# Performance work log

Measured on AMD Instinct MI355X. Metric: run time of the kernel, lower is better.

Reference implementation:

```python
import jax, jax.numpy as jnp
import numpy as np
import math

INPUT_DIM = 1024
EXPANSION = 4
SPARSITY = 0.15
ACT_SPARSITY = 0.1
OUTPUT_DIM = INPUT_DIM * EXPANSION
K = max(1, int(OUTPUT_DIM * ACT_SPARSITY))  # 409
BATCH = 16384


def setup_inputs() -> dict:
    key = jax.random.key(0)
    kx, kw, km = jax.random.split(key, 3)
    x = jax.random.normal(kx, (BATCH, INPUT_DIM), dtype=jnp.float32)
    # sparse random projection buffer, built exactly as in __init__
    w = jax.random.normal(kw, (OUTPUT_DIM, INPUT_DIM), dtype=jnp.float32)
    mask = (jax.random.uniform(km, (OUTPUT_DIM, INPUT_DIM)) < SPARSITY).astype(jnp.float32)
    scale = 1.5 / math.sqrt(INPUT_DIM * SPARSITY)
    projection_weights = w * mask * scale
    return {"x": x, "projection_weights": projection_weights}


def reference(x, projection_weights):
    # data-dependent bipolar rescale: torch uses `if x.min() >= 0`; express with where
    x_bipolar = jnp.where(x.min() >= 0, (x - 0.5) * 2.0, x)
    # [B, D_out] dense projection
    projected = jnp.einsum("bi,oi->bo", x_bipolar, projection_weights)
    # k-WTA: threshold at k-th largest value per row
    top_values, _ = jax.lax.top_k(projected, K)
    threshold = top_values[:, -1:]  # [B, 1]
    mask = (projected >= threshold).astype(projected.dtype)
    encoded = jax.nn.relu(projected) * mask
    # F.normalize(p=2, dim=1): divide by max(norm, eps)
    norm = jnp.sqrt(jnp.sum(encoded * encoded, axis=1, keepdims=True))
    return encoded / jnp.maximum(norm, 1e-12)
```

## Files before the change

kernel.cpp:

```cpp
#include <hip/hip_runtime.h>

#define BATCH   16384
#define IN_DIM  1024
#define OUT_DIM 4096
#define K_TOP   409
#define DELTA_W 6.5e-3f

typedef _Float16 half8  __attribute__((ext_vector_type(8)));
typedef _Float16 half4v __attribute__((ext_vector_type(4)));
typedef float    f32x4  __attribute__((ext_vector_type(4)));

#define WS_XH_OFF   256
#define WS_WH_OFF   (WS_XH_OFF + (size_t)BATCH * IN_DIM * 2)
#define WS_THR_OFF  (WS_WH_OFF + (size_t)OUT_DIM * IN_DIM * 2)
#define WS_CNT_OFF  (WS_THR_OFF + (size_t)BATCH * 8)
#define WS_COL_OFF  (WS_CNT_OFF + (size_t)BATCH * 8)
#define WS_NP_OFF   (WS_COL_OFF + (size_t)BATCH * 64 * 4)
#define WS_WV_OFF   (WS_NP_OFF + (size_t)BATCH * 64 * 4)
#define WS_WI_OFF   (WS_WV_OFF + (size_t)OUT_DIM * 256 * 4)
#define WS_WN_OFF   (WS_WI_OFF + (size_t)OUT_DIM * 256 * 2)
#define WS_NEEDED   (WS_WH_OFF + (size_t)OUT_DIM * IN_DIM * 2)
#define WS_NEED3    (WS_WN_OFF + (size_t)OUT_DIM * 4)


__global__ __launch_bounds__(256)
void k_hasneg(const float* __restrict__ x, int n, int* __restrict__ flag) {
    const int stride = gridDim.x * blockDim.x;
    bool neg = false;
    for (int i = blockIdx.x * blockDim.x + threadIdx.x; i < n; i += stride)
        neg |= (x[i] < 0.0f);
    unsigned long long b = __ballot(neg);
    if (b != 0ULL && (threadIdx.x & 63) == 0)
        atomicOr(flag, 1);
}

__global__ __launch_bounds__(256)
void k_cvt(const float* __restrict__ x, const float* __restrict__ w,
           _Float16* __restrict__ xh, _Float16* __restrict__ wh,
           const int* __restrict__ flag) {
    const bool bipolar = (*flag == 0);
    const int stride = gridDim.x * blockDim.x;
    const int nx4 = BATCH * IN_DIM / 4;
    const int nw4 = OUT_DIM * IN_DIM / 4;
    for (int i = blockIdx.x * blockDim.x + threadIdx.x; i < nx4; i += stride) {
        float4 v = ((const float4*)x)[i];
        if (bipolar) {
            v.x = (v.x - 0.5f) * 2.0f; v.y = (v.y - 0.5f) * 2.0f;
            v.z = (v.z - 0.5f) * 2.0f; v.w = (v.w - 0.5f) * 2.0f;
        }
        ((half4v*)xh)[i] = half4v{ (_Float16)v.x, (_Float16)v.y,
                                   (_Float16)v.z, (_Float16)v.w };
    }
    for (int i = blockIdx.x * blockDim.x + threadIdx.x; i < nw4; i += stride) {
        float4 u = ((const float4*)w)[i];
        ((half4v*)wh)[i] = half4v{ (_Float16)u.x, (_Float16)u.y,
                                   (_Float16)u.z, (_Float16)u.w };
    }
}

__global__ __launch_bounds__(256)
void k_wcomp(const float* __restrict__ w, float* __restrict__ wv,
             unsigned short* __restrict__ wi, int* __restrict__ wn) {
    const int lane = threadIdx.x & 63;
    const int row = blockIdx.x * 4 + (threadIdx.x >> 6);
    const float* wr = w + (size_t)row * IN_DIM;
    const float4* wr4 = (const float4*)(wr + lane * 16);
    float4 v[4];
    int cnt = 0;
    #pragma unroll
    for (int q = 0; q < 4; ++q) {
        v[q] = wr4[q];
        cnt += (v[q].x != 0.0f) + (v[q].y != 0.0f)
             + (v[q].z != 0.0f) + (v[q].w != 0.0f);
    }
    int off = cnt;
    #pragma unroll
    for (int d = 1; d < 64; d <<= 1) {
        int t = __shfl_up(off, d);
        if (lane >= d) off += t;
    }
    const int total = __shfl(off, 63);
    off -= cnt;
    float* dv = wv + (size_t)row * 256;
    unsigned short* di = wi + (size_t)row * 256;
    int pos = off;
    #pragma unroll
    for (int q = 0; q < 4; ++q) {
        #pragma unroll
        for (int e = 0; e < 4; ++e) {
            float f = (e == 0) ? v[q].x : (e == 1) ? v[q].y
                    : (e == 2) ? v[q].z : v[q].w;
            if (f != 0.0f) {
                dv[pos] = f;
                di[pos] = (unsigned short)(lane * 16 + q * 4 + e);
                ++pos;
            }
        }
    }
    if (lane == 0) {
        const int n4 = (total + 3) & ~3;
        for (int i = total; i < n4 && i < 256; ++i) { dv[i] = 0.0f; di[i] = 0; }
        wn[row] = total;
    }
}

__global__ __launch_bounds__(512, 2)
void k_gemm16(const _Float16* __restrict__ xh, const _Float16* __restrict__ wh,
              float* __restrict__ out) {
    __shared__ _Float16 Ah[2][256 * 64];
    __shared__ _Float16 Bh[2][256 * 64];
    const int tid = threadIdx.x;
    const int bm = blockIdx.x, bn = blockIdx.y;
    const int lane = tid & 63;
    const int wv = tid >> 6;
    const int wm = wv >> 2, wn = wv & 3;
    const int lr = lane & 15, lk = lane >> 4;

    const int srow = (lane >> 3);
    const int sslot = (lane & 7) ^ srow;
    f32x4 acc[8][4] = {};

    const _Float16* aS[4]; const _Float16* bS[4];
    int dOff[4];
    #pragma unroll
    for (int i = 0; i < 4; ++i) {
        const int rb = i * 64 + wv * 8;
        aS[i] = xh + (size_t)(bm * 256 + rb + srow) * IN_DIM + sslot * 8;
        bS[i] = wh + (size_t)(bn * 256 + rb + srow) * IN_DIM + sslot * 8;
        dOff[i] = rb * 64;
    }

    #pragma unroll
    for (int i = 0; i < 4; ++i) {
        __builtin_amdgcn_global_load_lds((const __attribute__((address_space(1))) void*)(aS[i]), (__attribute__((address_space(3))) void*)&Ah[0][dOff[i]], 16, 0, 0);
        __builtin_amdgcn_global_load_lds((const __attribute__((address_space(1))) void*)(bS[i]), (__attribute__((address_space(3))) void*)&Bh[0][dOff[i]], 16, 0, 0);
    }
    __syncthreads();

    int cur = 0;
    #pragma unroll 1
    for (int t = 0; t < 16; ++t) {
        if (t < 15) {
            const int kt = (t + 1) * 64;
            #pragma unroll
            for (int i = 0; i < 4; ++i) {
                __builtin_amdgcn_global_load_lds((const __attribute__((address_space(1))) void*)(aS[i] + kt), (__attribute__((address_space(3))) void*)&Ah[cur ^ 1][dOff[i]], 16, 0, 0);
                __builtin_amdgcn_global_load_lds((const __attribute__((address_space(1))) void*)(bS[i] + kt), (__attribute__((address_space(3))) void*)&Bh[cur ^ 1][dOff[i]], 16, 0, 0);
            }
        }
        #pragma unroll
        for (int h = 0; h < 2; ++h) {
            half8 bf[4];
            #pragma unroll
            for (int j = 0; j < 4; ++j) {
                const int rbv = wn * 64 + j * 16 + lr;
                const int sb = (h * 4 + lk) ^ (rbv & 7);
                bf[j] = *(const half8*)&Bh[cur][rbv * 64 + (sb << 3)];
            }
            #pragma unroll
            for (int hf = 0; hf < 2; ++hf) {
                half8 af[4];
                #pragma unroll
                for (int i = 0; i < 4; ++i) {
                    const int ra = wm * 128 + (hf * 4 + i) * 16 + lr;
                    const int sa = (h * 4 + lk) ^ (ra & 7);
                    af[i] = *(const half8*)&Ah[cur][ra * 64 + (sa << 3)];
                }
                #pragma unroll
                for (int i = 0; i < 4; ++i)
                    #pragma unroll
                    for (int j = 0; j < 4; ++j)
                        acc[hf * 4 + i][j] = __builtin_amdgcn_mfma_f32_16x16x32_f16(
                            af[i], bf[j], acc[hf * 4 + i][j], 0, 0, 0);
            }
        }
        __syncthreads();
        cur ^= 1;
    }
    #pragma unroll
    for (int i = 0; i < 8; ++i)
        #pragma unroll
        for (int j = 0; j < 4; ++j)
            #pragma unroll
            for (int q = 0; q < 4; ++q) {
                const int row = bm * 256 + wm * 128 + i * 16 + lk * 4 + q;
                const int col = bn * 256 + wn * 64 + j * 16 + lr;
                _Float16* fo = (_Float16*)((char*)out + (size_t)row * OUT_DIM * 4);
                fo[col] = (_Float16)acc[i][j][q];
            }
}

__global__ __launch_bounds__(256)
void k_sel1(const float* __restrict__ po, float2* __restrict__ thr,
            int2* __restrict__ cnt, int* __restrict__ rcol) {
    __shared__ unsigned int bins[256];
    __shared__ float fred[4];
    __shared__ unsigned int wsum[4];
    __shared__ int s_b, s_b2;
    __shared__ unsigned int s_hi, s_slot, s_hi1;
    const int row = blockIdx.x;
    const int tid = threadIdx.x;
    const int lane = tid & 63, wq = tid >> 6;
    const _Float16* fr = (const _Float16*)((const char*)po + (size_t)row * OUT_DIM * 4);

    half8 h0 = *(const half8*)&fr[tid * 8];
    half8 h1 = *(const half8*)&fr[2048 + tid * 8];
    float fv[16];
    float vmax = -1e30f;
    #pragma unroll
    for (int e = 0; e < 8; ++e) {
        fv[e] = (float)h0[e];
        fv[8 + e] = (float)h1[e];
        vmax = fmaxf(vmax, fmaxf(fv[e], fv[8 + e]));
    }
    #pragma unroll
    for (int off = 32; off > 0; off >>= 1)
        vmax = fmaxf(vmax, __shfl_xor(vmax, off));
    if (lane == 0) fred[wq] = vmax;
    bins[tid] = 0;
    if (tid == 0) { s_hi = 0; s_slot = 0; s_b = 0; s_b2 = 0; s_hi1 = 0; }
    __syncthreads();
    vmax = fmaxf(fmaxf(fmaxf(fred[0], fred[1]), fmaxf(fred[2], fred[3])), 1e-6f);
    const float scale1 = 256.0f / vmax;
    const float invscale1 = vmax * (1.0f / 256.0f);

    #pragma unroll
    for (int e = 0; e < 16; ++e) {
        float f = fv[e];
        if (f > 0.0f) {
            int b = (int)(f * scale1);
            if (b > 255) b = 255;
            atomicAdd(&bins[b], 1u);
        }
    }
    __syncthreads();
    {
        const unsigned int c = bins[255 - tid];
        unsigned int sc = c;
        #pragma unroll
        for (int off = 1; off < 64; off <<= 1) {
            unsigned int t2 = __shfl_up(sc, off);
            if (lane >= off) sc += t2;
        }
        if (lane == 63) wsum[wq] = sc;
        __syncthreads();
        for (int q = 0; q < wq; ++q) sc += wsum[q];
        if ((int)sc >= K_TOP && (int)(sc - c) < K_TOP) {
            s_b = 255 - tid;
            s_hi1 = sc - c;
        }
    }
    __syncthreads();
    const int b1 = s_b;
    const unsigned int hi1 = s_hi1;
    const float blo = (float)b1 * invscale1;
    const float scale2 = scale1 * 256.0f;
    const float s2w = invscale1 * (1.0f / 256.0f);

    bins[tid] = 0;
    __syncthreads();
    #pragma unroll
    for (int e = 0; e < 16; ++e) {
        float f = fv[e];
        if (f > 0.0f) {
            int b = (int)(f * scale1);
            if (b > 255) b = 255;
            if (b == b1) {
                int b2 = (int)((f - blo) * scale2);
                if (b2 < 0) b2 = 0;
                if (b2 > 255) b2 = 255;
                atomicAdd(&bins[b2], 1u);
            }
        }
    }
    __syncthreads();
    {
        const unsigned int c = bins[255 - tid];
        unsigned int sc = c;
        #pragma unroll
        for (int off = 1; off < 64; off <<= 1) {
            unsigned int t2 = __shfl_up(sc, off);
            if (lane >= off) sc += t2;
        }
        if (lane == 63) wsum[wq] = sc;
        __syncthreads();
        for (int q = 0; q < wq; ++q) sc += wsum[q];
        if ((int)(hi1 + sc) >= K_TOP && (int)(hi1 + sc - c) < K_TOP)
            s_b2 = 255 - tid;
    }
    __syncthreads();
    const float thi = blo + (float)(s_b2 + 1) * s2w + DELTA_W;
    const float tlo = blo + (float)s_b2 * s2w - DELTA_W;

    #pragma unroll
    for (int e = 0; e < 16; ++e) {
        float f = fv[e];
        if (f > thi) atomicAdd(&s_hi, 1u);
        else if (f >= tlo) {
            unsigned int p = atomicAdd(&s_slot, 1u);
            const int j = (e < 8) ? (tid * 8 + e) : (2048 + tid * 8 + e - 8);
            if (p < 64) rcol[row * 64 + p] = j;
        }
    }
    __syncthreads();
    if (tid == 0) {
        int nb = (int)s_slot;
        int krem = K_TOP - (int)s_hi;
        if (krem > nb) krem = nb;
        if (krem < 0) krem = 0;
        thr[row] = make_float2(thi, tlo);
        cnt[row] = make_int2(nb, krem);
    }
}

__global__ __launch_bounds__(256)
void k_sel2(const float* __restrict__ x, const float* __restrict__ wvals,
            const unsigned short* __restrict__ widx, const int* __restrict__ wn,
            const int2* __restrict__ cnt, const int* __restrict__ rcol,
            float* __restrict__ rnp, const int* __restrict__ flag) {
    __shared__ float xs[4][IN_DIM];
    const int tid = threadIdx.x;
    const int lane = tid & 63;
    const int wv = tid >> 6;
    const int row = blockIdx.x * 4 + wv;
    const bool bipolar = (*flag == 0);

    const float4* xr4 = (const float4*)(x + (size_t)row * IN_DIM);
    #pragma unroll
    for (int u = 0; u < 4; ++u) {
        float4 xv = xr4[lane + 64 * u];
        if (bipolar) {
            xv.x = __fmul_rn(__fadd_rn(xv.x, -0.5f), 2.0f);
            xv.y = __fmul_rn(__fadd_rn(xv.y, -0.5f), 2.0f);
            xv.z = __fmul_rn(__fadd_rn(xv.z, -0.5f), 2.0f);
            xv.w = __fmul_rn(__fadd_rn(xv.w, -0.5f), 2.0f);
        }
        ((float4*)xs[wv])[lane + 64 * u] = xv;
    }
    __syncthreads();

    int nb = cnt[row].x; if (nb > 64) nb = 64;
    if (lane < nb) {
        const int col = rcol[row * 64 + lane];
        const int n4 = (wn[col] + 3) >> 2;
        const float4* v4 = (const float4*)(wvals + (size_t)col * 256);
        const ushort4* i4 = (const ushort4*)(widx + (size_t)col * 256);
        const float* xr = xs[wv];
        float p = 0.0f;
        #pragma unroll 2
        for (int i = 0; i < n4; ++i) {
            float4 vv = v4[i];
            ushort4 ii = i4[i];
            p = __fmaf_rn(xr[ii.x], vv.x, p);
            p = __fmaf_rn(xr[ii.y], vv.y, p);
            p = __fmaf_rn(xr[ii.z], vv.z, p);
            p = __fmaf_rn(xr[ii.w], vv.w, p);
        }
        rnp[row * 64 + lane] = p;
    }
}

__global__ __launch_bounds__(256)
void k_sel2_full(const float* __restrict__ x, const float* __restrict__ w,
                 const int2* __restrict__ cnt, const int* __restrict__ rcol,
                 float* __restrict__ rnp, const int* __restrict__ flag) {
    __shared__ float xs[4][IN_DIM];
    const int tid = threadIdx.x;
    const int lane = tid & 63;
    const int wv = tid >> 6;
    const int row = blockIdx.x * 4 + wv;
    const bool bipolar = (*flag == 0);

    const float4* xr4 = (const float4*)(x + (size_t)row * IN_DIM);
    #pragma unroll
    for (int u = 0; u < 4; ++u) {
        float4 xv = xr4[lane + 64 * u];
        if (bipolar) {
            xv.x = __fmul_rn(__fadd_rn(xv.x, -0.5f), 2.0f);
            xv.y = __fmul_rn(__fadd_rn(xv.y, -0.5f), 2.0f);
            xv.z = __fmul_rn(__fadd_rn(xv.z, -0.5f), 2.0f);
            xv.w = __fmul_rn(__fadd_rn(xv.w, -0.5f), 2.0f);
        }
        ((float4*)xs[wv])[lane + 64 * u] = xv;
    }
    __syncthreads();

    int nb = cnt[row].x; if (nb > 64) nb = 64;
    if (lane < nb) {
        const int col = rcol[row * 64 + lane];
        const float4* wr4 = (const float4*)(w + (size_t)col * IN_DIM);
        const float4* xs4 = (const float4*)xs[wv];
        float p = 0.0f;
        #pragma unroll 4
        for (int i = 0; i < IN_DIM / 4; ++i) {
            float4 xv = xs4[i];
            float4 wvv = wr4[i];
            p = __fmaf_rn(xv.x, wvv.x, p);
            p = __fmaf_rn(xv.y, wvv.y, p);
            p = __fmaf_rn(xv.z, wvv.z, p);
            p = __fmaf_rn(xv.w, wvv.w, p);
        }
        rnp[row * 64 + lane] = p;
    }
}

__global__ __launch_bounds__(256)
void k_sel3(float* __restrict__ po, const float2* __restrict__ thr,
            const int2* __restrict__ cnt, const int* __restrict__ rcol,
            const float* __restrict__ rnp) {
    __shared__ int bcol[64];
    __shared__ float bnp[64];
    __shared__ unsigned char bsel[64];
    __shared__ float fred[4];
    const int row = blockIdx.x;
    const int tid = threadIdx.x;
    const int lane = tid & 63, wq = tid >> 6;
    const float2 th = thr[row];
    const int2 cn = cnt[row];
    const float thi = th.x, tlo = th.y;
    const int nb = cn.x, krem = cn.y;
    const int nbc = nb > 64 ? 64 : nb;
    const bool need = (nb != krem);

    const _Float16* fr = (const _Float16*)((const char*)po + (size_t)row * OUT_DIM * 4);
    half8 h0 = *(const half8*)&fr[tid * 8];
    half8 h1 = *(const half8*)&fr[2048 + tid * 8];

    if (tid < nbc) { bcol[tid] = rcol[row * 64 + tid]; bnp[tid] = rnp[row * 64 + tid]; }
    __syncthreads();
    if (tid < nbc) {
        const float v = bnp[tid];
        int gc = 0;
        for (int l = 0; l < nbc; ++l) gc += (bnp[l] > v);
        bsel[tid] = (gc < krem) ? 1 : 0;
    }
    __syncthreads();

    float ov[16];
    float nrm2 = 0.0f;
    #pragma unroll
    for (int e = 0; e < 16; ++e) {
        float f = (e < 8) ? (float)h0[e] : (float)h1[e - 8];
        const int j = (e < 8) ? (tid * 8 + e) : (2048 + tid * 8 + e - 8);
        bool sel = (f > thi);
        float val = f;
        if (!sel && f >= tlo) {
            if (!need) sel = true;
            else {
                for (int m = 0; m < nbc; ++m)
                    if (bcol[m] == j) {
                        sel = (bsel[m] != 0);
                        val = bnp[m];
                        break;
                    }
            }
        }
        float eo = (sel && val > 0.0f) ? val : 0.0f;
        ov[e] = eo;
        nrm2 += eo * eo;
    }
    #pragma unroll
    for (int off = 32; off > 0; off >>= 1)
        nrm2 += __shfl_xor(nrm2, off);
    if (lane == 0) fred[wq] = nrm2;
    __syncthreads();
    const float total = fred[0] + fred[1] + fred[2] + fred[3];
    const float inv = 1.0f / fmaxf(sqrtf(total), 1e-12f);

    float4* p4 = (float4*)(po + (size_t)row * OUT_DIM);
    #pragma unroll
    for (int h = 0; h < 2; ++h) {
        const int base = (h == 0) ? 0 : 8;
        const int fi = (h == 0) ? (tid * 2) : (512 + tid * 2);
        float4 o0 = make_float4(ov[base + 0] * inv, ov[base + 1] * inv,
                                ov[base + 2] * inv, ov[base + 3] * inv);
        float4 o1 = make_float4(ov[base + 4] * inv, ov[base + 5] * inv,
                                ov[base + 6] * inv, ov[base + 7] * inv);
        p4[fi] = o0;
        p4[fi + 1] = o1;
    }
}

extern "C" void kernel_launch(void* const* d_in, const int* in_sizes, int n_in,
                              void* d_out, int out_size, void* d_ws, size_t ws_size,
                              hipStream_t stream) {
    const float* x = (const float*)d_in[0];
    const float* w = (const float*)d_in[1];
    float* out = (float*)d_out;
    int* flag = (int*)d_ws;

    hipMemsetAsync(flag, 0, sizeof(int), stream);
    k_hasneg<<<2048, 256, 0, stream>>>(x, BATCH * IN_DIM, flag);

    dim3 g(BATCH / 256, OUT_DIM / 256);
    _Float16* xh = (_Float16*)((char*)d_ws + WS_XH_OFF);
    _Float16* wh = (_Float16*)((char*)d_ws + WS_WH_OFF);
    k_cvt<<<2048, 256, 0, stream>>>(x, w, xh, wh, flag);
    k_gemm16<<<g, 512, 0, stream>>>(xh, wh, out);

    float2* thr = (float2*)((char*)d_ws + WS_THR_OFF);
    int2*   cnt = (int2*)((char*)d_ws + WS_CNT_OFF);
    int*    rcol = (int*)((char*)d_ws + WS_COL_OFF);
    float*  rnp = (float*)((char*)d_ws + WS_NP_OFF);
    k_sel1<<<BATCH, 256, 0, stream>>>(out, thr, cnt, rcol);
    if (ws_size >= WS_NEED3) {
        float* wv = (float*)((char*)d_ws + WS_WV_OFF);
        unsigned short* wi = (unsigned short*)((char*)d_ws + WS_WI_OFF);
        int* wn = (int*)((char*)d_ws + WS_WN_OFF);
        k_wcomp<<<OUT_DIM / 4, 256, 0, stream>>>(w, wv, wi, wn);
        k_sel2<<<BATCH / 4, 256, 0, stream>>>(x, wv, wi, wn, cnt, rcol, rnp, flag);
    } else {
        k_sel2_full<<<BATCH / 4, 256, 0, stream>>>(x, w, cnt, rcol, rnp, flag);
    }
    k_sel3<<<BATCH, 256, 0, stream>>>(out, thr, cnt, rcol, rnp);
}
```

Baseline: 450.9 us.

## Fuse selection stages into one per-row kernel and merge conversion with weight compaction

Three post-GEMM kernels (threshold histogram, borderline fp32 recompute, final mask/normalize) are merged into a single per-row kernel. The fp16 row stays in registers and the candidate column lists stay in shared memory instead of going through workspace arrays. The conversion kernel now also builds the compacted sparse weight rows, which removes a separate launch. This saves two row re-reads and several launches per call. In exchange the fused kernel has a larger shared-memory footprint and divergent branches, and the borderline dot products now run one row per block instead of packing four rows per block.

```diff
diff --git a/kernel.cpp b/kernel.cpp
--- a/kernel.cpp
+++ b/kernel.cpp
@@ -12,14 +12,10 @@
 
 #define WS_XH_OFF   256
 #define WS_WH_OFF   (WS_XH_OFF + (size_t)BATCH * IN_DIM * 2)
-#define WS_THR_OFF  (WS_WH_OFF + (size_t)OUT_DIM * IN_DIM * 2)
-#define WS_CNT_OFF  (WS_THR_OFF + (size_t)BATCH * 8)
-#define WS_COL_OFF  (WS_CNT_OFF + (size_t)BATCH * 8)
-#define WS_NP_OFF   (WS_COL_OFF + (size_t)BATCH * 64 * 4)
-#define WS_WV_OFF   (WS_NP_OFF + (size_t)BATCH * 64 * 4)
+#define WS_WV_OFF   (WS_WH_OFF + (size_t)OUT_DIM * IN_DIM * 2)
 #define WS_WI_OFF   (WS_WV_OFF + (size_t)OUT_DIM * 256 * 4)
 #define WS_WN_OFF   (WS_WI_OFF + (size_t)OUT_DIM * 256 * 2)
-#define WS_NEEDED   (WS_WH_OFF + (size_t)OUT_DIM * IN_DIM * 2)
+#define WS_NEEDED   (WS_WV_OFF)
 #define WS_NEED3    (WS_WN_OFF + (size_t)OUT_DIM * 4)
 
 
@@ -35,72 +31,73 @@
 }
 
 __global__ __launch_bounds__(256)
-void k_cvt(const float* __restrict__ x, const float* __restrict__ w,
-           _Float16* __restrict__ xh, _Float16* __restrict__ wh,
-           const int* __restrict__ flag) {
+void k_cvt2(const float* __restrict__ x, const float* __restrict__ w,
+            _Float16* __restrict__ xh, _Float16* __restrict__ wh,
+            float* __restrict__ wv, unsigned short* __restrict__ wi,
+            int* __restrict__ wn, int use_csr, const int* __restrict__ flag) {
     const bool bipolar = (*flag == 0);
-    const int stride = gridDim.x * blockDim.x;
-    const int nx4 = BATCH * IN_DIM / 4;
-    const int nw4 = OUT_DIM * IN_DIM / 4;
-    for (int i = blockIdx.x * blockDim.x + threadIdx.x; i < nx4; i += stride) {
-        float4 v = ((const float4*)x)[i];
-        if (bipolar) {
-            v.x = (v.x - 0.5f) * 2.0f; v.y = (v.y - 0.5f) * 2.0f;
-            v.z = (v.z - 0.5f) * 2.0f; v.w = (v.w - 0.5f) * 2.0f;
-        }
-        ((half4v*)xh)[i] = half4v{ (_Float16)v.x, (_Float16)v.y,
-                                   (_Float16)v.z, (_Float16)v.w };
-    }
-    for (int i = blockIdx.x * blockDim.x + threadIdx.x; i < nw4; i += stride) {
-        float4 u = ((const float4*)w)[i];
-        ((half4v*)wh)[i] = half4v{ (_Float16)u.x, (_Float16)u.y,
-                                   (_Float16)u.z, (_Float16)u.w };
-    }
-}
-
-__global__ __launch_bounds__(256)
-void k_wcomp(const float* __restrict__ w, float* __restrict__ wv,
-             unsigned short* __restrict__ wi, int* __restrict__ wn) {
-    const int lane = threadIdx.x & 63;
-    const int row = blockIdx.x * 4 + (threadIdx.x >> 6);
-    const float* wr = w + (size_t)row * IN_DIM;
+    const int tid = threadIdx.x;
+    const int lane = tid & 63;
+    const int wrow = blockIdx.x * 4 + (tid >> 6);
+
+    const float* wr = w + (size_t)wrow * IN_DIM;
     const float4* wr4 = (const float4*)(wr + lane * 16);
+    _Float16* whr = wh + (size_t)wrow * IN_DIM + lane * 16;
     float4 v[4];
     int cnt = 0;
     #pragma unroll
     for (int q = 0; q < 4; ++q) {
         v[q] = wr4[q];
+        ((half4v*)whr)[q] = half4v{ (_Float16)v[q].x, (_Float16)v[q].y,
+                                    (_Float16)v[q].z, (_Float16)v[q].w };
         cnt += (v[q].x != 0.0f) + (v[q].y != 0.0f)
              + (v[q].z != 0.0f) + (v[q].w != 0.0f);
     }
-    int off = cnt;
-    #pragma unroll
-    for (int d = 1; d < 64; d <<= 1) {
-        int t = __shfl_up(off, d);
-        if (lane >= d) off += t;
-    }
-    const int total = __shfl(off, 63);
-    off -= cnt;
-    float* dv = wv + (size_t)row * 256;
-    unsigned short* di = wi + (size_t)row * 256;
-    int pos = off;
-    #pragma unroll
-    for (int q = 0; q < 4; ++q) {
-        #pragma unroll
-        for (int e = 0; e < 4; ++e) {
-            float f = (e == 0) ? v[q].x : (e == 1) ? v[q].y
-                    : (e == 2) ? v[q].z : v[q].w;
-            if (f != 0.0f) {
-                dv[pos] = f;
-                di[pos] = (unsigned short)(lane * 16 + q * 4 + e);
-                ++pos;
-            }
-        }
-    }
-    if (lane == 0) {
-        const int n4 = (total + 3) & ~3;
-        for (int i = total; i < n4 && i < 256; ++i) { dv[i] = 0.0f; di[i] = 0; }
-        wn[row] = total;
+    if (use_csr) {
+        int off = cnt;
+        #pragma unroll
+        for (int d = 1; d < 64; d <<= 1) {
+            int t = __shfl_up(off, d);
+            if (lane >= d) off += t;
+        }
+        const int total = __shfl(off, 63);
+        off -= cnt;
+        float* dv = wv + (size_t)wrow * 256;
+        unsigned short* di = wi + (size_t)wrow * 256;
+        int pos = off;
+        #pragma unroll
+        for (int q = 0; q < 4; ++q) {
+            #pragma unroll
+            for (int e = 0; e < 4; ++e) {
+                float f = (e == 0) ? v[q].x : (e == 1) ? v[q].y
+                        : (e == 2) ? v[q].z : v[q].w;
+                if (f != 0.0f) {
+                    dv[pos] = f;
+                    di[pos] = (unsigned short)(lane * 16 + q * 4 + e);
+                    ++pos;
+                }
+            }
+        }
+        if (lane == 0) {
+            const int n4 = (total + 3) & ~3;
+            for (int i = total; i < n4 && i < 256; ++i) { dv[i] = 0.0f; di[i] = 0; }
+            wn[wrow] = total;
+        }
+    }
+
+    const float4* x4 = (const float4*)x;
+    half4v* xh4 = (half4v*)xh;
+    const int base = blockIdx.x * 4096;
+    #pragma unroll
+    for (int u = 0; u < 16; ++u) {
+        const int idx = base + u * 256 + tid;
+        float4 xv = x4[idx];
+        if (bipolar) {
+            xv.x = (xv.x - 0.5f) * 2.0f; xv.y = (xv.y - 0.5f) * 2.0f;
+            xv.z = (xv.z - 0.5f) * 2.0f; xv.w = (xv.w - 0.5f) * 2.0f;
+        }
+        xh4[idx] = half4v{ (_Float16)xv.x, (_Float16)xv.y,
+                           (_Float16)xv.z, (_Float16)xv.w };
     }
 }
 
@@ -191,13 +188,21 @@
 }
 
 __global__ __launch_bounds__(256)
-void k_sel1(const float* __restrict__ po, float2* __restrict__ thr,
-            int2* __restrict__ cnt, int* __restrict__ rcol) {
+void k_self(float* __restrict__ po, const float* __restrict__ x,
+            const float* __restrict__ wvals, const unsigned short* __restrict__ widx,
+            const int* __restrict__ wn, const float* __restrict__ wfull,
+            int use_csr, const int* __restrict__ flag) {
     __shared__ unsigned int bins[256];
     __shared__ float fred[4];
     __shared__ unsigned int wsum[4];
+    __shared__ int ired[4];
     __shared__ int s_b, s_b2;
-    __shared__ unsigned int s_hi, s_slot, s_hi1;
+    __shared__ unsigned int s_slot, s_hi1;
+    __shared__ int bcol[64];
+    __shared__ float bnp[64];
+    __shared__ unsigned char bsel[64];
+    __shared__ float xs[IN_DIM];
+
     const int row = blockIdx.x;
     const int tid = threadIdx.x;
     const int lane = tid & 63, wq = tid >> 6;
@@ -218,7 +223,7 @@
         vmax = fmaxf(vmax, __shfl_xor(vmax, off));
     if (lane == 0) fred[wq] = vmax;
     bins[tid] = 0;
-    if (tid == 0) { s_hi = 0; s_slot = 0; s_b = 0; s_b2 = 0; s_hi1 = 0; }
+    if (tid == 0) { s_slot = 0; s_b = 0; s_b2 = 0; s_hi1 = 0; }
     __syncthreads();
     vmax = fmaxf(fmaxf(fmaxf(fred[0], fred[1]), fmaxf(fred[2], fred[3])), 1e-6f);
     const float scale1 = 256.0f / vmax;
@@ -292,155 +297,85 @@
     const float thi = blo + (float)(s_b2 + 1) * s2w + DELTA_W;
     const float tlo = blo + (float)s_b2 * s2w - DELTA_W;
 
+    int hic = 0;
     #pragma unroll
     for (int e = 0; e < 16; ++e) {
         float f = fv[e];
-        if (f > thi) atomicAdd(&s_hi, 1u);
+        if (f > thi) ++hic;
         else if (f >= tlo) {
             unsigned int p = atomicAdd(&s_slot, 1u);
             const int j = (e < 8) ? (tid * 8 + e) : (2048 + tid * 8 + e - 8);
-            if (p < 64) rcol[row * 64 + p] = j;
-        }
-    }
-    __syncthreads();
-    if (tid == 0) {
-        int nb = (int)s_slot;
-        int krem = K_TOP - (int)s_hi;
-        if (krem > nb) krem = nb;
-        if (krem < 0) krem = 0;
-        thr[row] = make_float2(thi, tlo);
-        cnt[row] = make_int2(nb, krem);
-    }
-}
-
-__global__ __launch_bounds__(256)
-void k_sel2(const float* __restrict__ x, const float* __restrict__ wvals,
-            const unsigned short* __restrict__ widx, const int* __restrict__ wn,
-            const int2* __restrict__ cnt, const int* __restrict__ rcol,
-            float* __restrict__ rnp, const int* __restrict__ flag) {
-    __shared__ float xs[4][IN_DIM];
-    const int tid = threadIdx.x;
-    const int lane = tid & 63;
-    const int wv = tid >> 6;
-    const int row = blockIdx.x * 4 + wv;
-    const bool bipolar = (*flag == 0);
-
-    const float4* xr4 = (const float4*)(x + (size_t)row * IN_DIM);
-    #pragma unroll
-    for (int u = 0; u < 4; ++u) {
-        float4 xv = xr4[lane + 64 * u];
+            if (p < 64) bcol[p] = j;
+        }
+    }
+    #pragma unroll
+    for (int off = 32; off > 0; off >>= 1)
+        hic += __shfl_xor(hic, off);
+    if (lane == 0) ired[wq] = hic;
+    __syncthreads();
+    const int hi = ired[0] + ired[1] + ired[2] + ired[3];
+    const int nb = (int)s_slot;
+    const int nbc = nb > 64 ? 64 : nb;
+    int krem = K_TOP - hi; if (krem > nb) krem = nb; if (krem < 0) krem = 0;
+    const bool need = (nb != krem);
+
+    if (need) {
+        const bool bipolar = (*flag == 0);
+        float4 xv = ((const float4*)(x + (size_t)row * IN_DIM))[tid];
         if (bipolar) {
             xv.x = __fmul_rn(__fadd_rn(xv.x, -0.5f), 2.0f);
             xv.y = __fmul_rn(__fadd_rn(xv.y, -0.5f), 2.0f);
             xv.z = __fmul_rn(__fadd_rn(xv.z, -0.5f), 2.0f);
             xv.w = __fmul_rn(__fadd_rn(xv.w, -0.5f), 2.0f);
         }
-        ((float4*)xs[wv])[lane + 64 * u] = xv;
-    }
-    __syncthreads();
-
-    int nb = cnt[row].x; if (nb > 64) nb = 64;
-    if (lane < nb) {
-        const int col = rcol[row * 64 + lane];
-        const int n4 = (wn[col] + 3) >> 2;
-        const float4* v4 = (const float4*)(wvals + (size_t)col * 256);
-        const ushort4* i4 = (const ushort4*)(widx + (size_t)col * 256);
-        const float* xr = xs[wv];
-        float p = 0.0f;
-        #pragma unroll 2
-        for (int i = 0; i < n4; ++i) {
-            float4 vv = v4[i];
-            ushort4 ii = i4[i];
-            p = __fmaf_rn(xr[ii.x], vv.x, p);
-            p = __fmaf_rn(xr[ii.y], vv.y, p);
-            p = __fmaf_rn(xr[ii.z], vv.z, p);
-            p = __fmaf_rn(xr[ii.w], vv.w, p);
-        }
-        rnp[row * 64 + lane] = p;
-    }
-}
-
-__global__ __launch_bounds__(256)
-void k_sel2_full(const float* __restrict__ x, const float* __restrict__ w,
-                 const int2* __restrict__ cnt, const int* __restrict__ rcol,
-                 float* __restrict__ rnp, const int* __restrict__ flag) {
-    __shared__ float xs[4][IN_DIM];
-    const int tid = threadIdx.x;
-    const int lane = tid & 63;
-    const int wv = tid >> 6;
-    const int row = blockIdx.x * 4 + wv;
-    const bool bipolar = (*flag == 0);
-
-    const float4* xr4 = (const float4*)(x + (size_t)row * IN_DIM);
-    #pragma unroll
-    for (int u = 0; u < 4; ++u) {
-        float4 xv = xr4[lane + 64 * u];
-        if (bipolar) {
-            xv.x = __fmul_rn(__fadd_rn(xv.x, -0.5f), 2.0f);
-            xv.y = __fmul_rn(__fadd_rn(xv.y, -0.5f), 2.0f);
-            xv.z = __fmul_rn(__fadd_rn(xv.z, -0.5f), 2.0f);
-            xv.w = __fmul_rn(__fadd_rn(xv.w, -0.5f), 2.0f);
-        }
-        ((float4*)xs[wv])[lane + 64 * u] = xv;
-    }
-    __syncthreads();
-
-    int nb = cnt[row].x; if (nb > 64) nb = 64;
-    if (lane < nb) {
-        const int col = rcol[row * 64 + lane];
-        const float4* wr4 = (const float4*)(w + (size_t)col * IN_DIM);
-        const float4* xs4 = (const float4*)xs[wv];
-        float p = 0.0f;
-        #pragma unroll 4
-        for (int i = 0; i < IN_DIM / 4; ++i) {
-            float4 xv = xs4[i];
-            float4 wvv = wr4[i];
-            p = __fmaf_rn(xv.x, wvv.x, p);
-            p = __fmaf_rn(xv.y, wvv.y, p);
-            p = __fmaf_rn(xv.z, wvv.z, p);
-            p = __fmaf_rn(xv.w, wvv.w, p);
-        }
-        rnp[row * 64 + lane] = p;
-    }
-}
-
-__global__ __launch_bounds__(256)
-void k_sel3(float* __restrict__ po, const float2* __restrict__ thr,
-            const int2* __restrict__ cnt, const int* __restrict__ rcol,
-            const float* __restrict__ rnp) {
-    __shared__ int bcol[64];
-    __shared__ float bnp[64];
-    __shared__ unsigned char bsel[64];
-    __shared__ float fred[4];
-    const int row = blockIdx.x;
-    const int tid = threadIdx.x;
-    const int lane = tid & 63, wq = tid >> 6;
-    const float2 th = thr[row];
-    const int2 cn = cnt[row];
-    const float thi = th.x, tlo = th.y;
-    const int nb = cn.x, krem = cn.y;
-    const int nbc = nb > 64 ? 64 : nb;
-    const bool need = (nb != krem);
-
-    const _Float16* fr = (const _Float16*)((const char*)po + (size_t)row * OUT_DIM * 4);
-    half8 h0 = *(const half8*)&fr[tid * 8];
-    half8 h1 = *(const half8*)&fr[2048 + tid * 8];
-
-    if (tid < nbc) { bcol[tid] = rcol[row * 64 + tid]; bnp[tid] = rnp[row * 64 + tid]; }
-    __syncthreads();
-    if (tid < nbc) {
-        const float v = bnp[tid];
-        int gc = 0;
-        for (int l = 0; l < nbc; ++l) gc += (bnp[l] > v);
-        bsel[tid] = (gc < krem) ? 1 : 0;
-    }
-    __syncthreads();
+        ((float4*)xs)[tid] = xv;
+        __syncthreads();
+        if (tid < nbc) {
+            const int col = bcol[tid];
+            float p = 0.0f;
+            if (use_csr) {
+                const int n4 = (wn[col] + 3) >> 2;
+                const float4* v4 = (const float4*)(wvals + (size_t)col * 256);
+                const ushort4* i4 = (const ushort4*)(widx + (size_t)col * 256);
+                #pragma unroll 2
+                for (int i = 0; i < n4; ++i) {
+                    float4 vv = v4[i];
+                    ushort4 ii = i4[i];
+                    p = __fmaf_rn(xs[ii.x], vv.x, p);
+                    p = __fmaf_rn(xs[ii.y], vv.y, p);
+                    p = __fmaf_rn(xs[ii.z], vv.z, p);
+                    p = __fmaf_rn(xs[ii.w], vv.w, p);
+                }
+            } else {
+                const float4* wr4 = (const float4*)(wfull + (size_t)col * IN_DIM);
+                const float4* xs4 = (const float4*)xs;
+                #pragma unroll 4
+                for (int i = 0; i < IN_DIM / 4; ++i) {
+                    float4 xq = xs4[i];
+                    float4 wq2 = wr4[i];
+                    p = __fmaf_rn(xq.x, wq2.x, p);
+                    p = __fmaf_rn(xq.y, wq2.y, p);
+                    p = __fmaf_rn(xq.z, wq2.z, p);
+                    p = __fmaf_rn(xq.w, wq2.w, p);
+                }
+            }
+            bnp[tid] = p;
+        }
+        __syncthreads();
+        if (tid < nbc) {
+            const float v = bnp[tid];
+            int gc = 0;
+            for (int l = 0; l < nbc; ++l) gc += (bnp[l] > v);
+            bsel[tid] = (gc < krem) ? 1 : 0;
+        }
+        __syncthreads();
+    }
 
     float ov[16];
     float nrm2 = 0.0f;
     #pragma unroll
     for (int e = 0; e < 16; ++e) {
-        float f = (e < 8) ? (float)h0[e] : (float)h1[e - 8];
+        float f = fv[e];
         const int j = (e < 8) ? (tid * 8 + e) : (2048 + tid * 8 + e - 8);
         bool sel = (f > thi);
         float val = f;
@@ -488,29 +423,21 @@
     const float* w = (const float*)d_in[1];
     float* out = (float*)d_out;
     int* flag = (int*)d_ws;
+    const int use_csr = (ws_size >= WS_NEED3) ? 1 : 0;
 
     hipMemsetAsync(flag, 0, sizeof(int), stream);
     k_hasneg<<<2048, 256, 0, stream>>>(x, BATCH * IN_DIM, flag);
 
-    dim3 g(BATCH / 256, OUT_DIM / 256);
     _Float16* xh = (_Float16*)((char*)d_ws + WS_XH_OFF);
     _Float16* wh = (_Float16*)((char*)d_ws + WS_WH_OFF);
-    k_cvt<<<2048, 256, 0, stream>>>(x, w, xh, wh, flag);
+    float* wv = (float*)((char*)d_ws + WS_WV_OFF);
+    unsigned short* wi = (unsigned short*)((char*)d_ws + WS_WI_OFF);
+    int* wn = (int*)((char*)d_ws + WS_WN_OFF);
+
+    k_cvt2<<<OUT_DIM / 4, 256, 0, stream>>>(x, w, xh, wh, wv, wi, wn,
+                                            use_csr, flag);
+    dim3 g(BATCH / 256, OUT_DIM / 256);
     k_gemm16<<<g, 512, 0, stream>>>(xh, wh, out);
 
-    float2* thr = (float2*)((char*)d_ws + WS_THR_OFF);
-    int2*   cnt = (int2*)((char*)d_ws + WS_CNT_OFF);
-    int*    rcol = (int*)((char*)d_ws + WS_COL_OFF);
-    float*  rnp = (float*)((char*)d_ws + WS_NP_OFF);
-    k_sel1<<<BATCH, 256, 0, stream>>>(out, thr, cnt, rcol);
-    if (ws_size >= WS_NEED3) {
-        float* wv = (float*)((char*)d_ws + WS_WV_OFF);
-        unsigned short* wi = (unsigned short*)((char*)d_ws + WS_WI_OFF);
-        int* wn = (int*)((char*)d_ws + WS_WN_OFF);
-        k_wcomp<<<OUT_DIM / 4, 256, 0, stream>>>(w, wv, wi, wn);
-        k_sel2<<<BATCH / 4, 256, 0, stream>>>(x, wv, wi, wn, cnt, rcol, rnp, flag);
-    } else {
-        k_sel2_full<<<BATCH / 4, 256, 0, stream>>>(x, w, cnt, rcol, rnp, flag);
-    }
-    k_sel3<<<BATCH, 256, 0, stream>>>(out, thr, cnt, rcol, rnp);
+    k_self<<<BATCH, 256, 0, stream>>>(out, x, wv, wi, wn, w, use_csr, flag);
 }
```

Result: faster. 438.3 us (-2.8%).
